# Optimization experiments

Hardware: AMD Instinct MI355X
Metric: run time of the kernel (lower is better)

The kernel has to match this reference:

```python
import jax, jax.numpy as jnp
import numpy as np

D, M = 64, 32            # feature dim, shapelet length
N_SEQ, SEG_LEN = 4096, 512
T = N_SEQ * SEG_LEN      # total concatenated length


def setup_inputs() -> dict:
    key = jax.random.key(0)
    k1, k2, k3, k4 = jax.random.split(key, 4)
    X = jax.random.normal(k1, (1, D, T), dtype=jnp.float32)
    query = jax.random.normal(k2, (1, D, M), dtype=jnp.float32)
    lin_w = jax.random.normal(k3, (2, 1), dtype=jnp.float32) * 0.5
    lin_b = jax.random.normal(k4, (2,), dtype=jnp.float32) * 0.1
    # cumsum of [0] + lens(X): equal-length segments here, but the kernel below
    # handles arbitrary ragged cumlens.
    cumlens = jnp.arange(N_SEQ + 1, dtype=jnp.int32) * SEG_LEN
    return {"X": X, "query": query, "lin_w": lin_w, "lin_b": lin_b, "cumlens": cumlens}


def reference(X, query, lin_w, lin_b, cumlens):
    m = query.shape[-1]
    n_seg = cumlens.shape[0] - 1
    dn = ('NCH', 'OIH', 'NCH')
    # sliding squared Euclidean distance: ||q||^2 + conv(x^2, 1) - 2*conv(x, q)
    ones_w = jnp.ones_like(query)
    QQ = jnp.sum(query * query)
    XX = jax.lax.conv_general_dilated(X * X, ones_w, (1,), 'VALID', dimension_numbers=dn)
    QX = jax.lax.conv_general_dilated(X, query, (1,), 'VALID', dimension_numbers=dn)
    dist = (QQ + XX - 2.0 * QX)[0, 0]          # [T - m + 1]
    P = dist.shape[0]
    pos = jnp.arange(P)
    # segment id of each window start; windows crossing a segment boundary
    # (start > cumlens[i+1] - m) are excluded, matching Dist[c_i : c_{i+1}-m+1]
    seg = jnp.searchsorted(cumlens, pos, side='right') - 1
    valid = pos <= (cumlens[seg + 1] - m)
    BIG = jnp.float32(1e30)
    masked = jnp.where(valid, dist, BIG)
    mins = jax.ops.segment_min(masked, seg, num_segments=n_seg)   # [N]
    # MinMaxscaler with UpdateMinMax=True
    lo, hi = jnp.min(mins), jnp.max(mins)
    scaled = (mins - lo) / (hi - lo + 1e-16)
    # Linear(1, 2)
    return scaled[:, None] @ lin_w.T + lin_b   # [N, 2]
```

## Files before the change

### kernel.cpp

```cpp
#include <hip/hip_runtime.h>

#define D_FEAT 64
#define M_LEN 32
#define BLOCK 512
#define MAXSEG 512
#define HALF_J 16
#define CHUNK 8
#define BIGF 1e30f

__global__ __launch_bounds__(BLOCK, 4) void seg_min_kernel(
    const float* __restrict__ X, const float* __restrict__ q,
    const int* __restrict__ cumlens, float* __restrict__ mins, long long T)
{
    __shared__ float h[HALF_J * MAXSEG];

    const int seg  = blockIdx.x;
    const int base = cumlens[seg];
    const int len  = cumlens[seg + 1] - base;
    const int tid  = threadIdx.x;
    const int col  = tid < len ? tid : (len > 0 ? len - 1 : 0);

    float c[M_LEN];
    #pragma unroll
    for (int j = 0; j < M_LEN; ++j) c[j] = 0.0f;
    float xx = 0.0f;

    const float* xp = X + (size_t)base + (size_t)col;

    float vb3[3][CHUNK];
    #pragma unroll
    for (int b = 0; b < 3; ++b)
        #pragma unroll
        for (int dd = 0; dd < CHUNK; ++dd)
            vb3[b][dd] = __builtin_nontemporal_load(
                xp + (size_t)(b * CHUNK + dd) * (size_t)T);

    #pragma unroll
    for (int k = 0; k < D_FEAT / CHUNK; ++k) {
        #pragma unroll
        for (int dd = 0; dd < CHUNK; ++dd) {
            const float x = vb3[k % 3][dd];
            xx = fmaf(x, x, xx);
            const float* __restrict__ qd = q + (k * CHUNK + dd) * M_LEN;
            #pragma unroll
            for (int j = 0; j < M_LEN; ++j)
                c[j] = fmaf(x, qd[j], c[j]);
        }
        if (k + 3 < D_FEAT / CHUNK) {
            #pragma unroll
            for (int dd = 0; dd < CHUNK; ++dd)
                vb3[k % 3][dd] = __builtin_nontemporal_load(
                    xp + (size_t)((k + 3) * CHUNK + dd) * (size_t)T);
        }
    }

    #pragma unroll
    for (int j = 0; j < HALF_J; ++j)
        h[j * MAXSEG + col] = fmaf(-2.0f, c[j], xx);
    __syncthreads();

    const bool valid = (tid + M_LEN - 1 < len);
    float acc = 0.0f;
    if (valid) {
        #pragma unroll
        for (int j = 0; j < HALF_J; ++j)
            acc += h[j * MAXSEG + tid + j];
    }
    __syncthreads();

    #pragma unroll
    for (int j = HALF_J; j < M_LEN; ++j)
        h[(j - HALF_J) * MAXSEG + col] = fmaf(-2.0f, c[j], xx);
    __syncthreads();

    float dist = BIGF;
    if (valid) {
        #pragma unroll
        for (int j = HALF_J; j < M_LEN; ++j)
            acc += h[(j - HALF_J) * MAXSEG + tid + j];
        dist = acc;
    }

    #pragma unroll
    for (int off = 32; off > 0; off >>= 1)
        dist = fminf(dist, __shfl_down(dist, off));

    __syncthreads();
    if ((tid & 63) == 0) h[tid >> 6] = dist;
    __syncthreads();
    if (tid == 0) {
        float m = h[0];
        #pragma unroll
        for (int w = 1; w < BLOCK / 64; ++w) m = fminf(m, h[w]);
        mins[seg] = m;
    }
}

__global__ __launch_bounds__(1024) void finalize_kernel(
    const float* __restrict__ mins, const float* __restrict__ lw,
    const float* __restrict__ lb, float* __restrict__ out, int nseg)
{
    __shared__ float slo[16], shi[16];
    const int tid = threadIdx.x;
    float lo = BIGF, hi = -BIGF;
    for (int i = tid; i < nseg; i += blockDim.x) {
        float v = mins[i];
        lo = fminf(lo, v);
        hi = fmaxf(hi, v);
    }
    #pragma unroll
    for (int off = 32; off > 0; off >>= 1) {
        lo = fminf(lo, __shfl_down(lo, off));
        hi = fmaxf(hi, __shfl_down(hi, off));
    }
    const int nw = blockDim.x >> 6;
    if ((tid & 63) == 0) { slo[tid >> 6] = lo; shi[tid >> 6] = hi; }
    __syncthreads();
    if (tid == 0) {
        float l = slo[0], h2 = shi[0];
        for (int w = 1; w < nw; ++w) { l = fminf(l, slo[w]); h2 = fmaxf(h2, shi[w]); }
        slo[0] = l; shi[0] = h2;
    }
    __syncthreads();
    lo = slo[0]; hi = shi[0];
    const float inv = 1.0f / (hi - lo + 1e-16f);
    const float w0 = lw[0], w1 = lw[1], b0 = lb[0], b1 = lb[1];
    for (int i = tid; i < nseg; i += blockDim.x) {
        float s = (mins[i] - lo) * inv;
        out[2 * i]     = fmaf(s, w0, b0);
        out[2 * i + 1] = fmaf(s, w1, b1);
    }
}

extern "C" void kernel_launch(void* const* d_in, const int* in_sizes, int n_in,
                              void* d_out, int out_size, void* d_ws, size_t ws_size,
                              hipStream_t stream) {
    const float* X   = (const float*)d_in[0];
    const float* q   = (const float*)d_in[1];
    const float* lw  = (const float*)d_in[2];
    const float* lb  = (const float*)d_in[3];
    const int*   cum = (const int*)d_in[4];

    const int n_seg = in_sizes[4] - 1;
    const long long T = (long long)in_sizes[0] / D_FEAT;

    float* mins = (float*)d_ws;
    float* out  = (float*)d_out;

    seg_min_kernel<<<n_seg, BLOCK, 0, stream>>>(X, q, cum, mins, T);
    finalize_kernel<<<1, 1024, 0, stream>>>(mins, lw, lb, out, n_seg);
}
```

Before: 726.6 us.

## Compute two adjacent positions per thread with float2 loads and shared q reads

Halves the block size and has each thread process two consecutive window positions, loading X as float2 and reusing each q value for two FMAs. Per-thread register use doubles for the accumulator arrays. The explicit triple-buffered nontemporal prefetch is replaced with a non-unrolled loop over channel chunks. The aim is to amortize the q loads (uniform/scalar) and the address math over twice the work and to issue wider memory loads, at the risk of lower occupancy and less latency hiding. Odd segment lengths or segments longer than 512 could mishandle positions, and float2 alignment depends on base being even.

```diff
diff --git a/kernel.cpp b/kernel.cpp
--- a/kernel.cpp
+++ b/kernel.cpp
@@ -2,7 +2,7 @@
 
 #define D_FEAT 64
 #define M_LEN 32
-#define BLOCK 512
+#define BLOCK 256
 #define MAXSEG 512
 #define HALF_J 16
 #define CHUNK 8
@@ -18,67 +18,77 @@
     const int base = cumlens[seg];
     const int len  = cumlens[seg + 1] - base;
     const int tid  = threadIdx.x;
-    const int col  = tid < len ? tid : (len > 0 ? len - 1 : 0);
 
-    float c[M_LEN];
+    int p0 = 2 * tid;
+    if (p0 > len - 2) p0 = (len >= 2) ? (len - 2) : 0;
+
+    float c0[M_LEN], c1[M_LEN];
     #pragma unroll
-    for (int j = 0; j < M_LEN; ++j) c[j] = 0.0f;
-    float xx = 0.0f;
+    for (int j = 0; j < M_LEN; ++j) { c0[j] = 0.0f; c1[j] = 0.0f; }
+    float xx0 = 0.0f, xx1 = 0.0f;
 
-    const float* xp = X + (size_t)base + (size_t)col;
+    const float* xp = X + (size_t)base + (size_t)p0;
 
-    float vb3[3][CHUNK];
-    #pragma unroll
-    for (int b = 0; b < 3; ++b)
+    #pragma unroll 1
+    for (int d0 = 0; d0 < D_FEAT; d0 += CHUNK) {
+        float2 xv[CHUNK];
         #pragma unroll
         for (int dd = 0; dd < CHUNK; ++dd)
-            vb3[b][dd] = __builtin_nontemporal_load(
-                xp + (size_t)(b * CHUNK + dd) * (size_t)T);
+            xv[dd] = *reinterpret_cast<const float2*>(
+                xp + (size_t)(d0 + dd) * (size_t)T);
 
-    #pragma unroll
-    for (int k = 0; k < D_FEAT / CHUNK; ++k) {
         #pragma unroll
         for (int dd = 0; dd < CHUNK; ++dd) {
-            const float x = vb3[k % 3][dd];
-            xx = fmaf(x, x, xx);
-            const float* __restrict__ qd = q + (k * CHUNK + dd) * M_LEN;
+            const float x0 = xv[dd].x, x1 = xv[dd].y;
+            xx0 = fmaf(x0, x0, xx0);
+            xx1 = fmaf(x1, x1, xx1);
+            const float* __restrict__ qd = q + (d0 + dd) * M_LEN;
             #pragma unroll
-            for (int j = 0; j < M_LEN; ++j)
-                c[j] = fmaf(x, qd[j], c[j]);
-        }
-        if (k + 3 < D_FEAT / CHUNK) {
-            #pragma unroll
-            for (int dd = 0; dd < CHUNK; ++dd)
-                vb3[k % 3][dd] = __builtin_nontemporal_load(
-                    xp + (size_t)((k + 3) * CHUNK + dd) * (size_t)T);
+            for (int j = 0; j < M_LEN; ++j) {
+                const float qv = qd[j];
+                c0[j] = fmaf(x0, qv, c0[j]);
+                c1[j] = fmaf(x1, qv, c1[j]);
+            }
         }
     }
 
     #pragma unroll
-    for (int j = 0; j < HALF_J; ++j)
-        h[j * MAXSEG + col] = fmaf(-2.0f, c[j], xx);
+    for (int j = 0; j < HALF_J; ++j) {
+        h[j * MAXSEG + p0]     = fmaf(-2.0f, c0[j], xx0);
+        h[j * MAXSEG + p0 + 1] = fmaf(-2.0f, c1[j], xx1);
+    }
     __syncthreads();
 
-    const bool valid = (tid + M_LEN - 1 < len);
-    float acc = 0.0f;
-    if (valid) {
+    const bool v0 = (p0 + M_LEN - 1 < len);
+    const bool v1 = (p0 + M_LEN     < len);
+    float a0 = 0.0f, a1 = 0.0f;
+    if (v0) {
         #pragma unroll
-        for (int j = 0; j < HALF_J; ++j)
-            acc += h[j * MAXSEG + tid + j];
+        for (int j = 0; j < HALF_J; ++j) a0 += h[j * MAXSEG + p0 + j];
+    }
+    if (v1) {
+        #pragma unroll
+        for (int j = 0; j < HALF_J; ++j) a1 += h[j * MAXSEG + p0 + 1 + j];
     }
     __syncthreads();
 
     #pragma unroll
-    for (int j = HALF_J; j < M_LEN; ++j)
-        h[(j - HALF_J) * MAXSEG + col] = fmaf(-2.0f, c[j], xx);
+    for (int j = HALF_J; j < M_LEN; ++j) {
+        h[(j - HALF_J) * MAXSEG + p0]     = fmaf(-2.0f, c0[j], xx0);
+        h[(j - HALF_J) * MAXSEG + p0 + 1] = fmaf(-2.0f, c1[j], xx1);
+    }
     __syncthreads();
 
     float dist = BIGF;
-    if (valid) {
+    if (v0) {
         #pragma unroll
-        for (int j = HALF_J; j < M_LEN; ++j)
-            acc += h[(j - HALF_J) * MAXSEG + tid + j];
-        dist = acc;
+        for (int j = HALF_J; j < M_LEN; ++j) a0 += h[(j - HALF_J) * MAXSEG + p0 + j];
+        dist = a0;
+    }
+    if (v1) {
+        #pragma unroll
+        for (int j = HALF_J; j < M_LEN; ++j) a1 += h[(j - HALF_J) * MAXSEG + p0 + 1 + j];
+        dist = fminf(dist, a1);
     }
 
     #pragma unroll
```

Result: faster. 691.8 us (-4.8%).
